# Optimization experiments

Hardware: AMD Instinct MI355X
Metric: run time of the kernel (lower is better)

The kernel has to match this reference:

```python
import jax, jax.numpy as jnp
import numpy as np

ANCHORS = np.array([[10.0, 13.0], [16.0, 30.0], [33.0, 23.0]], dtype=np.float32)
IMG_SIZE = 416.0
NUM_CLASSES = 80
IGNORE_THR = 0.5
LAMBDA_XY, LAMBDA_WH, LAMBDA_CONF, LAMBDA_CLS = 1.0, 1.0, 5.0, 1.0
EPS = 1e-12


def setup_inputs() -> dict:
    key = jax.random.key(0)
    k1, k2, k3 = jax.random.split(key, 3)
    bs, A, nc, H, W, T = 32, 3, NUM_CLASSES, 52, 52, 50
    inp = jax.random.normal(k1, (bs, A * (5 + nc), H, W), dtype=jnp.float32)
    cls = jax.random.randint(k2, (bs, T, 1), 0, nc).astype(jnp.float32)
    coords = jax.random.uniform(k3, (bs, T, 4), minval=0.02, maxval=0.98, dtype=jnp.float32)
    targets = jnp.concatenate([cls, coords], axis=-1)  # (class, cx, cy, w, h), normalized
    return {"input": inp, "targets": targets}


def _bce(p, t):
    # elementwise binary cross entropy, sum-reduced by caller; torch convention 0*log(0)=0
    return -(t * jnp.log(jnp.clip(p, EPS, 1.0)) + (1.0 - t) * jnp.log(jnp.clip(1.0 - p, EPS, 1.0)))


def reference(input, targets):
    bs, _, H, W = input.shape
    anchors_px = jnp.asarray(ANCHORS)              # [A,2] in image pixels
    A = anchors_px.shape[0]
    nc = NUM_CLASSES
    stride = IMG_SIZE / H                          # square grid assumed (as in source)
    anchors = anchors_px / stride                  # scaled anchors [A,2]

    pred = input.reshape(bs, A, 5 + nc, H, W).transpose(0, 1, 3, 4, 2)  # [bs,A,H,W,5+nc]
    x = jax.nn.sigmoid(pred[..., 0])
    y = jax.nn.sigmoid(pred[..., 1])
    w = pred[..., 2]
    h = pred[..., 3]
    conf = jax.nn.sigmoid(pred[..., 4])
    pred_cls = jax.nn.sigmoid(pred[..., 5:])

    grid_x = jnp.arange(W, dtype=jnp.float32)[None, None, None, :]
    grid_y = jnp.arange(H, dtype=jnp.float32)[None, None, :, None]
    aw = anchors[:, 0][None, :, None, None]
    ah = anchors[:, 1][None, :, None, None]
    # pred boxes are detached in the original (uses .data)
    px = jax.lax.stop_gradient(x) + grid_x
    py = jax.lax.stop_gradient(y) + grid_y
    pw = jnp.exp(jax.lax.stop_gradient(w)) * aw
    ph = jnp.exp(jax.lax.stop_gradient(h)) * ah

    # ---- vectorized get_target ----
    targets = jax.lax.stop_gradient(targets)
    T = targets.shape[1]
    valid = jnp.sum(targets, axis=-1) > 0          # [bs,T]
    gx = targets[..., 1] * W
    gy = targets[..., 2] * H
    gw = targets[..., 3] * W
    gh = targets[..., 4] * H
    gi = jnp.clip(gx.astype(jnp.int32), 0, W - 1)  # [bs,T]
    gj = jnp.clip(gy.astype(jnp.int32), 0, H - 1)

    # anchor matching: wh-IoU at a common center
    inter_a = jnp.minimum(gw[..., None], anchors[:, 0]) * jnp.minimum(gh[..., None], anchors[:, 1])
    union_a = (gw * gh)[..., None] + anchors[:, 0] * anchors[:, 1] - inter_a
    anch_iou = inter_a / (union_a + 1e-16)         # [bs,T,A]
    best_n = jnp.argmax(anch_iou, axis=-1)         # [bs,T]

    # gt vs all predicted boxes (center-format IoU): [bs,T,A,H,W]
    b1x1 = (gx - gw / 2)[:, :, None, None, None]
    b1x2 = (gx + gw / 2)[:, :, None, None, None]
    b1y1 = (gy - gh / 2)[:, :, None, None, None]
    b1y2 = (gy + gh / 2)[:, :, None, None, None]
    b2x1 = (px - pw / 2)[:, None]
    b2x2 = (px + pw / 2)[:, None]
    b2y1 = (py - ph / 2)[:, None]
    b2y2 = (py + ph / 2)[:, None]
    iw = jnp.clip(jnp.minimum(b1x2, b2x2) - jnp.maximum(b1x1, b2x1), 0.0)
    ih = jnp.clip(jnp.minimum(b1y2, b2y2) - jnp.maximum(b1y1, b2y1), 0.0)
    inter_p = iw * ih
    area1 = (gw * gh)[:, :, None, None, None]
    area2 = (pw * ph)[:, None]
    pred_iou = inter_p / (area1 + area2 - inter_p + 1e-16)  # [bs,T,A,H,W]

    ignore = jnp.any((pred_iou >= IGNORE_THR) & valid[:, :, None, None, None], axis=1)
    noobj_mask = jnp.where(ignore, 0.0, 1.0)       # [bs,A,H,W]

    # scatter targets into the best (anchor, cell) of each gt box; invalid rows dropped
    b_idx = jnp.broadcast_to(jnp.arange(bs)[:, None], (bs, T))
    t_idx = jnp.broadcast_to(jnp.arange(T)[None, :], (bs, T))
    gi_s = jnp.where(valid, gi, W).reshape(-1)     # out-of-range -> mode='drop'
    bf = b_idx.reshape(-1)
    nf = best_n.reshape(-1)
    jf = gj.reshape(-1)

    zeros4 = jnp.zeros((bs, A, H, W), dtype=jnp.float32)
    mask = zeros4.at[bf, nf, jf, gi_s].set(1.0, mode='drop')
    noobj_mask = noobj_mask.at[bf, nf, jf, gi_s].set(0.0, mode='drop')
    tx = zeros4.at[bf, nf, jf, gi_s].set((gx - gi.astype(jnp.float32)).reshape(-1), mode='drop')
    ty = zeros4.at[bf, nf, jf, gi_s].set((gy - gj.astype(jnp.float32)).reshape(-1), mode='drop')
    tw_val = jnp.log(gw / anchors[best_n, 0] + 1e-16)
    th_val = jnp.log(gh / anchors[best_n, 1] + 1e-16)
    tw = zeros4.at[bf, nf, jf, gi_s].set(tw_val.reshape(-1), mode='drop')
    th = zeros4.at[bf, nf, jf, gi_s].set(th_val.reshape(-1), mode='drop')
    tconf_val = pred_iou[b_idx, t_idx, best_n, gj, gi]  # [bs,T] (stored but unused by losses)
    tconf = zeros4.at[bf, nf, jf, gi_s].set(tconf_val.reshape(-1), mode='drop')
    cls_f = jnp.clip(targets[..., 0].astype(jnp.int32), 0, nc - 1).reshape(-1)
    tcls = jnp.zeros((bs, A, H, W, nc), dtype=jnp.float32).at[bf, nf, jf, gi_s, cls_f].set(1.0, mode='drop')

    n_obj = jnp.maximum(jnp.sum(valid.astype(jnp.float32)), 1.0)

    # ---- losses (sum-reduced, as nn.MSELoss/BCELoss(size_average=False)) ----
    loss_x = jnp.sum((x * mask - tx * mask) ** 2) / (2 * n_obj)
    loss_y = jnp.sum((y * mask - ty * mask) ** 2) / (2 * n_obj)
    loss_w = jnp.sum((w * mask - tw * mask) ** 2) / (2 * n_obj)
    loss_h = jnp.sum((h * mask - th * mask) ** 2) / (2 * n_obj)
    # bce(conf*mask, mask): zero where mask==0 (bce(0,0)=0), -log(conf) where mask==1
    loss_conf_obj = -jnp.sum(mask * jnp.log(jnp.clip(conf, EPS, 1.0)))
    # bce(conf*noobj, 0): -log(1-conf) where noobj==1, zero elsewhere
    loss_conf_noobj = -jnp.sum(noobj_mask * jnp.log(jnp.clip(1.0 - conf, EPS, 1.0)))
    loss_conf = loss_conf_obj / n_obj + 0.2 * loss_conf_noobj / n_obj
    loss_cls = jnp.sum(mask[..., None] * _bce(pred_cls, tcls)) / n_obj

    loss = (loss_x * LAMBDA_XY + loss_y * LAMBDA_XY + loss_w * LAMBDA_WH + loss_h * LAMBDA_WH
            + loss_conf * LAMBDA_CONF + loss_cls * LAMBDA_CLS)

    # global_step < 12800 branch (early anchor-prior loss), always applied here
    a_loss = (jnp.sum((x - 0.5) ** 2) + jnp.sum((y - 0.5) ** 2)
              + jnp.sum(w ** 2) + jnp.sum(h ** 2)) / (2 * n_obj)
    loss = loss + 0.1 * a_loss
    return loss
```

## Files before the change

kernel.cpp:

```cpp
#include <hip/hip_runtime.h>
#include <math.h>

#define BS 32
#define NA 3
#define NC 80
#define HH 52
#define WW 52
#define TPER 50
#define NTT (BS * TPER)
#define HW (HH * WW)
#define CPB (NA * HW)
#define CH (5 + NC)
#define CELLS_PER_BLK 1024
#define CBPB 8
#define NCELLBLK (BS * CBPB)
#define OBJ_PAIRS 25
#define NOBJBLK (BS * OBJ_PAIRS)
#define NBLK (NCELLBLK + NOBJBLK)

__device__ __forceinline__ float fexp(float x) { return __builtin_amdgcn_exp2f(x * 1.4426950408889634f); }
__device__ __forceinline__ float flog(float x) { return __builtin_amdgcn_logf(x) * 0.6931471805599453f; }
__device__ __forceinline__ float sigm(float v) { return __builtin_amdgcn_rcpf(1.0f + fexp(-v)); }

__device__ __forceinline__ float wave_red(float t) {
    #pragma unroll
    for (int off = 32; off > 0; off >>= 1) t += __shfl_down(t, off);
    return t;
}


__global__ __launch_bounds__(256) void k_main(const float* __restrict__ in,
                                              const float* __restrict__ tgt,
                                              float2* __restrict__ ws)
{
    __shared__ float4 sbox[TPER];
    __shared__ unsigned sbm[CELLS_PER_BLK / 32];
    __shared__ float wred[4];
    const int tid = threadIdx.x;
    const float aw[3] = {1.25f, 2.0f, 4.125f};
    const float ah[3] = {1.625f, 3.75f, 2.875f};
    const float raw[3] = {0.8f, 0.5f, 0.24242424242424243f};
    const float rah[3] = {0.6153846153846154f, 0.26666666666666666f, 0.34782608695652173f};

    float term = 0.0f;
    float flag = 0.0f;

    if (blockIdx.x < NCELLBLK) {
        const int b  = blockIdx.x >> 3;
        const int lo = (blockIdx.x & 7) * CELLS_PER_BLK;
        if (tid < CELLS_PER_BLK / 32) sbm[tid] = 0u;
        int mycell = -1;
        if (tid < TPER) {
            const float* p = tgt + (size_t)(b * TPER + tid) * 5;
            float c0 = p[0], c1 = p[1], c2 = p[2], c3 = p[3], c4 = p[4];
            bool valid = (c0 + c1 + c2 + c3 + c4) > 0.0f;
            float gx = c1 * WW, gy = c2 * HH, gw = c3 * WW, gh = c4 * HH;
            int gi = (int)gx; gi = gi < 0 ? 0 : (gi > WW - 1 ? WW - 1 : gi);
            int gj = (int)gy; gj = gj < 0 ? 0 : (gj > HH - 1 ? HH - 1 : gj);
            int bn = 0;
            {
                float bi = fminf(gw, aw[0]) * fminf(gh, ah[0]);
                float bu = gw * gh + aw[0] * ah[0] - bi;
                #pragma unroll
                for (int a = 1; a < 3; ++a) {
                    float ia = fminf(gw, aw[a]) * fminf(gh, ah[a]);
                    float ua = gw * gh + aw[a] * ah[a] - ia;
                    if (ia * bu > bi * ua) { bn = a; bi = ia; bu = ua; }
                }
            }
            if (valid) {
                sbox[tid] = make_float4(gx - 0.5f * gw, gx + 0.5f * gw,
                                        gy - 0.5f * gh, gy + 0.5f * gh);
                mycell = bn * HW + gj * WW + gi;
            } else {
                sbox[tid] = make_float4(1e30f, 1e30f, 1e30f, 1e30f);
            }
        }
        __syncthreads();
        if (mycell >= lo && mycell < lo + CELLS_PER_BLK)
            atomicOr(&sbm[(mycell - lo) >> 5], 1u << ((mycell - lo) & 31));
        __syncthreads();

        const int q0 = lo + 4 * tid;
        const bool actq = q0 < CPB;
        float P1[4], P2[4], Q1[4], Q2[4], A2[4], CF[4];
        bool IGN[4] = {false, false, false, false};
        #pragma unroll
        for (int k = 0; k < 4; ++k) { P1[k]=0; P2[k]=0; Q1[k]=0; Q2[k]=0; A2[k]=1e30f; CF[k]=0.5f; }
        if (actq) {
            const int a  = q0 / HW;
            const int r  = q0 - a * HW;
            const int yy = r / WW;
            const int xx0 = r - yy * WW;
            const float* plane = in + ((size_t)b * (NA * CH) + a * CH) * HW + r;
            float4 X = *(const float4*)(plane);
            float4 Y = *(const float4*)(plane + HW);
            float4 Wv = *(const float4*)(plane + 2 * HW);
            float4 Hv = *(const float4*)(plane + 3 * HW);
            float4 Cv = *(const float4*)(plane + 4 * HW);
            float xs[4] = {X.x, X.y, X.z, X.w};
            float ys[4] = {Y.x, Y.y, Y.z, Y.w};
            float zs[4] = {Wv.x, Wv.y, Wv.z, Wv.w};
            float hs[4] = {Hv.x, Hv.y, Hv.z, Hv.w};
            float cs[4] = {Cv.x, Cv.y, Cv.z, Cv.w};
            #pragma unroll
            for (int k = 0; k < 4; ++k) {
                float sx = sigm(xs[k]), sy = sigm(ys[k]);
                CF[k] = sigm(cs[k]);
                float px = sx + (float)(xx0 + k), py = sy + (float)yy;
                float pw = fexp(zs[k]) * aw[a], ph = fexp(hs[k]) * ah[a];
                P1[k] = px - 0.5f * pw; P2[k] = px + 0.5f * pw;
                Q1[k] = py - 0.5f * ph; Q2[k] = py + 0.5f * ph;
                A2[k] = pw * ph + 1e-16f;
                term += 0.05f * ((sx - 0.5f) * (sx - 0.5f) + (sy - 0.5f) * (sy - 0.5f)
                                 + zs[k] * zs[k] + hs[k] * hs[k]);
            }
        }
        #pragma unroll 2
        for (int t = 0; t < TPER; ++t) {
            float4 bx = sbox[t];
            float ar = (bx.y - bx.x) * (bx.w - bx.z);
            #pragma unroll
            for (int k = 0; k < 4; ++k) {
                float iw = fmaxf(fminf(bx.y, P2[k]) - fmaxf(bx.x, P1[k]), 0.0f);
                float ih = fmaxf(fminf(bx.w, Q2[k]) - fmaxf(bx.z, Q1[k]), 0.0f);
                float inter = iw * ih;
                IGN[k] = IGN[k] || (3.0f * inter >= ar + A2[k]);
            }
        }
        if (actq) {
            #pragma unroll
            for (int k = 0; k < 4; ++k) {
                int d = 4 * tid + k;
                bool ist = (sbm[d >> 5] >> (d & 31)) & 1u;
                if (!IGN[k] && !ist)
                    term += -flog(fmaxf(1.0f - CF[k], 1e-12f));
            }
        }
    } else {
        const int o = blockIdx.x - NCELLBLK;
        const int b = o / OBJ_PAIRS;
        const int pair = o - b * OBJ_PAIRS;
        const int tA = 2 * pair;
        const int lane = tid & 63;
        const int wid = tid >> 6;
        const int myT = tA + (wid >> 1);
        const int k = ((wid & 1) << 6) | lane;

        int celll = -1, clsl = 0;
        if (lane < TPER) {
            const float* p = tgt + (size_t)(b * TPER + lane) * 5;
            float c0 = p[0], c1 = p[1], c2 = p[2], c3 = p[3], c4 = p[4];
            bool valid = (c0 + c1 + c2 + c3 + c4) > 0.0f;
            float gx = c1 * WW, gy = c2 * HH, gw = c3 * WW, gh = c4 * HH;
            int gi = (int)gx; gi = gi < 0 ? 0 : (gi > WW - 1 ? WW - 1 : gi);
            int gj = (int)gy; gj = gj < 0 ? 0 : (gj > HH - 1 ? HH - 1 : gj);
            int bn = 0;
            {
                float bi = fminf(gw, aw[0]) * fminf(gh, ah[0]);
                float bu = gw * gh + aw[0] * ah[0] - bi;
                #pragma unroll
                for (int a = 1; a < 3; ++a) {
                    float ia = fminf(gw, aw[a]) * fminf(gh, ah[a]);
                    float ua = gw * gh + aw[a] * ah[a] - ia;
                    if (ia * bu > bi * ua) { bn = a; bi = ia; bu = ua; }
                }
            }
            celll = valid ? (bn * HW + gj * WW + gi) : -1;
            int cls = (int)c0; cls = cls < 0 ? 0 : (cls > NC - 1 ? NC - 1 : cls);
            clsl = cls;
        }
        const int cell = __shfl(celll, myT);
        bool mt = (lane < TPER) && (cell >= 0) && (celll == cell);
        unsigned long long mask = __ballot(mt);
        bool owner = (cell >= 0) && ((mask >> (myT + 1)) == 0ULL);
        int a = 0, r = 0;
        float v = 0.0f;
        if (cell >= 0 && k < 85) {
            a = cell / HW;
            r = cell - a * HW;
            v = in[((size_t)b * (NA * CH) + a * CH + k) * HW + r];
        }
        if (owner && k < 85) {
            if (k < 5) {
                const float* p = tgt + (size_t)(b * TPER + myT) * 5;
                if (k == 0) {
                    float gx = p[1] * WW; int gi = r - (r / WW) * WW;
                    float d = sigm(v) - (gx - (float)gi); term = 0.5f * d * d;
                } else if (k == 1) {
                    float gy = p[2] * HH; int gj = r / WW;
                    float d = sigm(v) - (gy - (float)gj); term = 0.5f * d * d;
                } else if (k == 2) {
                    float d = v - flog(p[3] * WW * raw[a] + 1e-16f); term = 0.5f * d * d;
                } else if (k == 3) {
                    float d = v - flog(p[4] * HH * rah[a] + 1e-16f); term = 0.5f * d * d;
                } else {
                    term = -5.0f * flog(fmaxf(sigm(v), 1e-12f));
                }
            } else {
                int c = k - 5;
                bool pos = false;
                unsigned long long mm = mask;
                while (mm) {
                    int t2 = __ffsll(mm) - 1; mm &= mm - 1;
                    pos = pos || (__shfl(clsl, t2) == c);
                }
                float p = sigm(v);
                term = pos ? -flog(fmaxf(p, 1e-12f)) : -flog(fmaxf(1.0f - p, 1e-12f));
            }
        }
        int cA = __shfl(celll, tA), cB = __shfl(celll, tA + 1);
        flag = (cA >= 0 ? 1.0f : 0.0f) + (cB >= 0 ? 1.0f : 0.0f);
    }

    float tr = wave_red(term);
    if ((tid & 63) == 0) wred[tid >> 6] = tr;
    __syncthreads();
    if (tid == 0)
        ws[blockIdx.x] = make_float2(wred[0] + wred[1] + wred[2] + wred[3], flag);
}

__global__ __launch_bounds__(256) void k_final(const float2* __restrict__ ws,
                                               float* __restrict__ out)
{
    const int tid = threadIdx.x;
    const float4* w4 = (const float4*)ws;
    float s = 0.0f, nv = 0.0f;
    for (int i = tid; i < NBLK / 2; i += 256) {
        float4 v = w4[i];
        s += v.x + v.z;
        nv += v.y + v.w;
    }
    __shared__ float wr0[4], wr1[4];
    s = wave_red(s);
    nv = wave_red(nv);
    if ((tid & 63) == 0) { wr0[tid >> 6] = s; wr1[tid >> 6] = nv; }
    __syncthreads();
    if (tid == 0) {
        float S = wr0[0] + wr0[1] + wr0[2] + wr0[3];
        float N = wr1[0] + wr1[1] + wr1[2] + wr1[3];
        out[0] = S / fmaxf(N, 1.0f);
    }
}

extern "C" void kernel_launch(void* const* d_in, const int* in_sizes, int n_in,
                              void* d_out, int out_size, void* d_ws, size_t ws_size,
                              hipStream_t stream)
{
    const float* in = (const float*)d_in[0];
    const float* tgt = (const float*)d_in[1];
    float2* ws = (float2*)d_ws;

    k_main<<<NBLK, 256, 0, stream>>>(in, tgt, ws);
    k_final<<<1, 256, 0, stream>>>(ws, (float*)d_out);
}
```

Before: 17.50 us.

## Halve cells per thread, pack one object per wave, slim final reduction

Cell blocks now cover 512 cells with two cells per thread instead of four, doubling the block count for better CU coverage while still repeating the per-box IoU loop for each cell. Object blocks handle four targets per block, one per wave, with each lane loading two channels so all 85 channels fit in one wave. The final reduction kernel uses a single wave and drops the shared-memory stage. The risk is extra duplicated target preprocessing and the loss of float4 loads.

```diff
diff --git a/kernel.cpp b/kernel.cpp
--- a/kernel.cpp
+++ b/kernel.cpp
@@ -11,11 +11,11 @@
 #define HW (HH * WW)
 #define CPB (NA * HW)
 #define CH (5 + NC)
-#define CELLS_PER_BLK 1024
-#define CBPB 8
+#define CELLS_PER_BLK 512
+#define CBPB 16
 #define NCELLBLK (BS * CBPB)
-#define OBJ_PAIRS 25
-#define NOBJBLK (BS * OBJ_PAIRS)
+#define OBJ_QPB 13
+#define NOBJBLK (BS * OBJ_QPB)
 #define NBLK (NCELLBLK + NOBJBLK)
 
 __device__ __forceinline__ float fexp(float x) { return __builtin_amdgcn_exp2f(x * 1.4426950408889634f); }
@@ -46,8 +46,8 @@
     float flag = 0.0f;
 
     if (blockIdx.x < NCELLBLK) {
-        const int b  = blockIdx.x >> 3;
-        const int lo = (blockIdx.x & 7) * CELLS_PER_BLK;
+        const int b  = blockIdx.x >> 4;
+        const int lo = (blockIdx.x & 15) * CELLS_PER_BLK;
         if (tid < CELLS_PER_BLK / 32) sbm[tid] = 0u;
         int mycell = -1;
         if (tid < TPER) {
@@ -81,30 +81,30 @@
             atomicOr(&sbm[(mycell - lo) >> 5], 1u << ((mycell - lo) & 31));
         __syncthreads();
 
-        const int q0 = lo + 4 * tid;
+        const int q0 = lo + 2 * tid;
         const bool actq = q0 < CPB;
-        float P1[4], P2[4], Q1[4], Q2[4], A2[4], CF[4];
-        bool IGN[4] = {false, false, false, false};
+        float P1[2], P2[2], Q1[2], Q2[2], A2[2], CF[2];
+        bool IGN[2] = {false, false};
         #pragma unroll
-        for (int k = 0; k < 4; ++k) { P1[k]=0; P2[k]=0; Q1[k]=0; Q2[k]=0; A2[k]=1e30f; CF[k]=0.5f; }
+        for (int k = 0; k < 2; ++k) { P1[k]=0; P2[k]=0; Q1[k]=0; Q2[k]=0; A2[k]=1e30f; CF[k]=0.5f; }
         if (actq) {
             const int a  = q0 / HW;
             const int r  = q0 - a * HW;
             const int yy = r / WW;
             const int xx0 = r - yy * WW;
             const float* plane = in + ((size_t)b * (NA * CH) + a * CH) * HW + r;
-            float4 X = *(const float4*)(plane);
-            float4 Y = *(const float4*)(plane + HW);
-            float4 Wv = *(const float4*)(plane + 2 * HW);
-            float4 Hv = *(const float4*)(plane + 3 * HW);
-            float4 Cv = *(const float4*)(plane + 4 * HW);
-            float xs[4] = {X.x, X.y, X.z, X.w};
-            float ys[4] = {Y.x, Y.y, Y.z, Y.w};
-            float zs[4] = {Wv.x, Wv.y, Wv.z, Wv.w};
-            float hs[4] = {Hv.x, Hv.y, Hv.z, Hv.w};
-            float cs[4] = {Cv.x, Cv.y, Cv.z, Cv.w};
-            #pragma unroll
-            for (int k = 0; k < 4; ++k) {
+            float2 X = *(const float2*)(plane);
+            float2 Y = *(const float2*)(plane + HW);
+            float2 Wv = *(const float2*)(plane + 2 * HW);
+            float2 Hv = *(const float2*)(plane + 3 * HW);
+            float2 Cv = *(const float2*)(plane + 4 * HW);
+            float xs[2] = {X.x, X.y};
+            float ys[2] = {Y.x, Y.y};
+            float zs[2] = {Wv.x, Wv.y};
+            float hs[2] = {Hv.x, Hv.y};
+            float cs[2] = {Cv.x, Cv.y};
+            #pragma unroll
+            for (int k = 0; k < 2; ++k) {
                 float sx = sigm(xs[k]), sy = sigm(ys[k]);
                 CF[k] = sigm(cs[k]);
                 float px = sx + (float)(xx0 + k), py = sy + (float)yy;
@@ -121,7 +121,7 @@
             float4 bx = sbox[t];
             float ar = (bx.y - bx.x) * (bx.w - bx.z);
             #pragma unroll
-            for (int k = 0; k < 4; ++k) {
+            for (int k = 0; k < 2; ++k) {
                 float iw = fmaxf(fminf(bx.y, P2[k]) - fmaxf(bx.x, P1[k]), 0.0f);
                 float ih = fmaxf(fminf(bx.w, Q2[k]) - fmaxf(bx.z, Q1[k]), 0.0f);
                 float inter = iw * ih;
@@ -130,8 +130,8 @@
         }
         if (actq) {
             #pragma unroll
-            for (int k = 0; k < 4; ++k) {
-                int d = 4 * tid + k;
+            for (int k = 0; k < 2; ++k) {
+                int d = 2 * tid + k;
                 bool ist = (sbm[d >> 5] >> (d & 31)) & 1u;
                 if (!IGN[k] && !ist)
                     term += -flog(fmaxf(1.0f - CF[k], 1e-12f));
@@ -139,13 +139,12 @@
         }
     } else {
         const int o = blockIdx.x - NCELLBLK;
-        const int b = o / OBJ_PAIRS;
-        const int pair = o - b * OBJ_PAIRS;
-        const int tA = 2 * pair;
+        const int b = o / OBJ_QPB;
+        const int quad = o - b * OBJ_QPB;
+        const int tA = 4 * quad;
         const int lane = tid & 63;
         const int wid = tid >> 6;
-        const int myT = tA + (wid >> 1);
-        const int k = ((wid & 1) << 6) | lane;
+        const int myT = tA + wid;
 
         int celll = -1, clsl = 0;
         if (lane < TPER) {
@@ -175,42 +174,60 @@
         unsigned long long mask = __ballot(mt);
         bool owner = (cell >= 0) && ((mask >> (myT + 1)) == 0ULL);
         int a = 0, r = 0;
-        float v = 0.0f;
-        if (cell >= 0 && k < 85) {
+        float v1 = 0.0f, v2 = 0.0f;
+        if (cell >= 0) {
             a = cell / HW;
             r = cell - a * HW;
-            v = in[((size_t)b * (NA * CH) + a * CH + k) * HW + r];
-        }
-        if (owner && k < 85) {
-            if (k < 5) {
+            const float* bp = in + ((size_t)b * (NA * CH) + a * CH) * HW + r;
+            v1 = bp[(size_t)lane * HW];
+            if (lane < CH - 64) v2 = bp[(size_t)(lane + 64) * HW];
+        }
+        if (owner) {
+            if (lane < 5) {
                 const float* p = tgt + (size_t)(b * TPER + myT) * 5;
-                if (k == 0) {
+                if (lane == 0) {
                     float gx = p[1] * WW; int gi = r - (r / WW) * WW;
-                    float d = sigm(v) - (gx - (float)gi); term = 0.5f * d * d;
-                } else if (k == 1) {
+                    float d = sigm(v1) - (gx - (float)gi); term = 0.5f * d * d;
+                } else if (lane == 1) {
                     float gy = p[2] * HH; int gj = r / WW;
-                    float d = sigm(v) - (gy - (float)gj); term = 0.5f * d * d;
-                } else if (k == 2) {
-                    float d = v - flog(p[3] * WW * raw[a] + 1e-16f); term = 0.5f * d * d;
-                } else if (k == 3) {
-                    float d = v - flog(p[4] * HH * rah[a] + 1e-16f); term = 0.5f * d * d;
+                    float d = sigm(v1) - (gy - (float)gj); term = 0.5f * d * d;
+                } else if (lane == 2) {
+                    float d = v1 - flog(p[3] * WW * raw[a] + 1e-16f); term = 0.5f * d * d;
+                } else if (lane == 3) {
+                    float d = v1 - flog(p[4] * HH * rah[a] + 1e-16f); term = 0.5f * d * d;
                 } else {
-                    term = -5.0f * flog(fmaxf(sigm(v), 1e-12f));
+                    term = -5.0f * flog(fmaxf(sigm(v1), 1e-12f));
                 }
-            } else {
-                int c = k - 5;
-                bool pos = false;
-                unsigned long long mm = mask;
-                while (mm) {
-                    int t2 = __ffsll(mm) - 1; mm &= mm - 1;
-                    pos = pos || (__shfl(clsl, t2) == c);
-                }
-                float p = sigm(v);
-                term = pos ? -flog(fmaxf(p, 1e-12f)) : -flog(fmaxf(1.0f - p, 1e-12f));
-            }
-        }
-        int cA = __shfl(celll, tA), cB = __shfl(celll, tA + 1);
-        flag = (cA >= 0 ? 1.0f : 0.0f) + (cB >= 0 ? 1.0f : 0.0f);
+            }
+            int c1 = lane - 5;
+            int c2 = lane + 59;
+            bool pos1 = false, pos2 = false;
+            unsigned long long mm = mask;
+            while (mm) {
+                int t2 = __ffsll(mm) - 1; mm &= mm - 1;
+                int cc = __shfl(clsl, t2);
+                pos1 = pos1 || (cc == c1);
+                pos2 = pos2 || (cc == c2);
+            }
+            if (lane >= 5) {
+                float p = sigm(v1);
+                term = pos1 ? -flog(fmaxf(p, 1e-12f)) : -flog(fmaxf(1.0f - p, 1e-12f));
+            }
+            if (lane < CH - 64) {
+                float p = sigm(v2);
+                term += pos2 ? -flog(fmaxf(p, 1e-12f)) : -flog(fmaxf(1.0f - p, 1e-12f));
+            }
+        }
+        if (wid == 0) {
+            float f = 0.0f;
+            #pragma unroll
+            for (int j = 0; j < 4; ++j) {
+                int tj = tA + j;
+                int cj = (tj < TPER) ? __shfl(celll, tj) : -1;
+                f += (cj >= 0) ? 1.0f : 0.0f;
+            }
+            flag = f;
+        }
     }
 
     float tr = wave_red(term);
@@ -220,27 +237,20 @@
         ws[blockIdx.x] = make_float2(wred[0] + wred[1] + wred[2] + wred[3], flag);
 }
 
-__global__ __launch_bounds__(256) void k_final(const float2* __restrict__ ws,
-                                               float* __restrict__ out)
+__global__ __launch_bounds__(64) void k_final(const float2* __restrict__ ws,
+                                              float* __restrict__ out)
 {
     const int tid = threadIdx.x;
     const float4* w4 = (const float4*)ws;
     float s = 0.0f, nv = 0.0f;
-    for (int i = tid; i < NBLK / 2; i += 256) {
+    for (int i = tid; i < NBLK / 2; i += 64) {
         float4 v = w4[i];
         s += v.x + v.z;
         nv += v.y + v.w;
     }
-    __shared__ float wr0[4], wr1[4];
     s = wave_red(s);
     nv = wave_red(nv);
-    if ((tid & 63) == 0) { wr0[tid >> 6] = s; wr1[tid >> 6] = nv; }
-    __syncthreads();
-    if (tid == 0) {
-        float S = wr0[0] + wr0[1] + wr0[2] + wr0[3];
-        float N = wr1[0] + wr1[1] + wr1[2] + wr1[3];
-        out[0] = S / fmaxf(N, 1.0f);
-    }
+    if (tid == 0) out[0] = s / fmaxf(nv, 1.0f);
 }
 
 extern "C" void kernel_launch(void* const* d_in, const int* in_sizes, int n_in,
@@ -252,5 +262,5 @@
     float2* ws = (float2*)d_ws;
 
     k_main<<<NBLK, 256, 0, stream>>>(in, tgt, ws);
-    k_final<<<1, 256, 0, stream>>>(ws, (float*)d_out);
-}
+    k_final<<<1, 64, 0, stream>>>(ws, (float*)d_out);
+}
```

New measurement: 18.44 us. 1.05x slower.
